# Kernel tuning notes

Hardware: AMD Instinct MI355X
Metric: run time of the kernel (lower is better)

The kernel has to match this reference:

```python
import jax, jax.numpy as jnp
import numpy as np

N = 1_000_000
C = 128
NBINS = 15


def setup_inputs() -> dict:
    key = jax.random.key(0)
    k1, k2 = jax.random.split(key)
    logits = jax.random.normal(k1, (N, C), dtype=jnp.float32)
    labels = jax.random.randint(k2, (N,), 0, C, dtype=jnp.int64)
    return {"logits": logits, "labels": labels}


def reference(logits, labels):
    n = logits.shape[0]
    probs = jax.nn.softmax(logits, axis=1)
    confidences = jnp.max(probs, axis=1)                      # [N]
    predictions = jnp.argmax(probs, axis=1)                   # [N]
    accuracies = (predictions == labels).astype(jnp.float32)  # [N]

    # Equal-count (adaptive) bin edges: interp(linspace(0,N,nbins+1), arange(N), sort(conf))
    sorted_conf = jnp.sort(confidences)
    q = jnp.linspace(0.0, float(n), NBINS + 1)
    edges = jnp.interp(q, jnp.arange(n, dtype=jnp.float32), sorted_conf)  # [NBINS+1]

    # Bin i covers (edges[i], edges[i+1]] to match conf.gt(lower) & conf.le(upper).
    idx = jnp.searchsorted(edges[1:-1], confidences, side="left")  # [N] in [0, NBINS-1]
    valid = (confidences > edges[0]) & (confidences <= edges[-1])
    idx = jnp.where(valid, idx, NBINS)  # dump out-of-range into extra segment

    cnt = jax.ops.segment_sum(jnp.ones_like(confidences), idx, num_segments=NBINS + 1)[:NBINS]
    csum = jax.ops.segment_sum(confidences, idx, num_segments=NBINS + 1)[:NBINS]
    asum = jax.ops.segment_sum(accuracies, idx, num_segments=NBINS + 1)[:NBINS]

    prop = cnt / jnp.float32(n)
    safe = jnp.maximum(cnt, 1.0)
    gap = jnp.abs(csum / safe - asum / safe)
    ece = jnp.sum(jnp.where(cnt > 0, gap * prop, 0.0))
    return ece.reshape(1)
```

## Files before the change

kernel.cpp:

```cpp
#include <hip/hip_runtime.h>
#include <hip/hip_bf16.h>
#include <cstdint>

#define NROWS 1000000
#define NCLS  128
#define NBINS 15

#define FBASE 0x3B000000u
#define NB    73728
#define SCAN_T 1024
#define PER   (NB / SCAN_T)

#define OFF_CONF   0u
#define OFF_ACC    4000000u
#define OFF_HIST   5000000u
#define OFF_SUB    5294912u
#define OFF_BINS   5417792u
#define OFF_TGTB   5418152u
#define OFF_TGTL   5418272u
#define OFF_EDGES  5418392u
#define ZERO_BYTES (OFF_TGTB - OFF_HIST)

#define ROWS_PER_BLOCK 32

__device__ __forceinline__ void reduce_row(float4 v0, float4 v1, int l16,
                                           float& c_out, int& mi_out)
{
    const int b0 = l16 * 4, b1 = 64 + l16 * 4;
    float m = v0.x; int mi = b0;
    if (v0.y > m) { m = v0.y; mi = b0 + 1; }
    if (v0.z > m) { m = v0.z; mi = b0 + 2; }
    if (v0.w > m) { m = v0.w; mi = b0 + 3; }
    if (v1.x > m) { m = v1.x; mi = b1; }
    if (v1.y > m) { m = v1.y; mi = b1 + 1; }
    if (v1.z > m) { m = v1.z; mi = b1 + 2; }
    if (v1.w > m) { m = v1.w; mi = b1 + 3; }
#pragma unroll
    for (int d = 1; d < 16; d <<= 1) {
        float om = __shfl_xor(m, d);
        int   oi = __shfl_xor(mi, d);
        if (om > m || (om == m && oi < mi)) { m = om; mi = oi; }
    }
    float s = __expf(v0.x - m) + __expf(v0.y - m) + __expf(v0.z - m) + __expf(v0.w - m)
            + __expf(v1.x - m) + __expf(v1.y - m) + __expf(v1.z - m) + __expf(v1.w - m);
#pragma unroll
    for (int d = 1; d < 16; d <<= 1) s += __shfl_xor(s, d);
    c_out  = 1.0f / s;
    mi_out = mi;
}

__global__ __launch_bounds__(256) void k_row(const float* __restrict__ logits,
                                             const int* __restrict__ labels,
                                             float* __restrict__ conf,
                                             unsigned char* __restrict__ acc,
                                             unsigned int* __restrict__ hist)
{
    const int wave = threadIdx.x >> 6;
    const int lane = threadIdx.x & 63;
    const int sub  = lane >> 4;
    const int l16  = lane & 15;
    const long long base = (long long)blockIdx.x * ROWS_PER_BLOCK + wave * 8;
    const long long rowA = base + sub;
    const long long rowB = base + 4 + sub;

    const float4* pA = reinterpret_cast<const float4*>(logits + rowA * NCLS);
    const float4* pB = reinterpret_cast<const float4*>(logits + rowB * NCLS);
    const float4 a0 = pA[l16];
    const float4 a1 = pA[16 + l16];
    const float4 b0 = pB[l16];
    const float4 b1 = pB[16 + l16];
    const int labA = labels[rowA];
    const int labB = labels[rowB];

    float cA, cB; int miA, miB;
    reduce_row(a0, a1, l16, cA, miA);
    reduce_row(b0, b1, l16, cB, miB);

    if (l16 == 0) {
        conf[rowA] = cA;
        acc[rowA]  = (labA == miA) ? 1u : 0u;
        int ubA = (int)(__float_as_uint(cA) - FBASE);
        int bA  = ubA >> 10;
        bA = bA < 0 ? 0 : (bA >= NB ? NB - 1 : bA);
        atomicAdd(&hist[bA], 1u);

        conf[rowB] = cB;
        acc[rowB]  = (labB == miB) ? 1u : 0u;
        int ubB = (int)(__float_as_uint(cB) - FBASE);
        int bB  = ubB >> 10;
        bB = bB < 0 ? 0 : (bB >= NB ? NB - 1 : bB);
        atomicAdd(&hist[bB], 1u);
    }
}

__device__ __forceinline__ unsigned int rank_of(int s)
{
    if (s == 0)  return 0u;
    if (s == 29) return (unsigned int)(NROWS - 1);
    int i = (s + 1) >> 1;
    unsigned int k = (unsigned int)((long long)i * NROWS / 15);
    return k + ((s & 1) ? 0u : 1u);
}

__global__ __launch_bounds__(SCAN_T) void k_scan(const unsigned int* __restrict__ hist,
                                                 int* __restrict__ tgtb,
                                                 int* __restrict__ tgtl)
{
    __shared__ unsigned int v[SCAN_T];
    const int t = threadIdx.x;
    unsigned int s = 0;
    for (int j = 0; j < PER; j++) s += hist[t * PER + j];
    v[t] = s;
    __syncthreads();
    for (int off = 1; off < SCAN_T; off <<= 1) {
        unsigned int x = (t >= off) ? v[t - off] : 0u;
        __syncthreads();
        v[t] += x;
        __syncthreads();
    }
    const unsigned int run0 = v[t] - s;
    for (int s2 = 0; s2 < 30; s2++) {
        unsigned int r = rank_of(s2);
        if (r >= run0 && r < run0 + s) {
            unsigned int run = run0;
            for (int j = 0; j < PER; j++) {
                unsigned int c = hist[t * PER + j];
                if (r < run + c) { tgtb[s2] = t * PER + j; tgtl[s2] = (int)(r - run); break; }
                run += c;
            }
        }
    }
}

__global__ __launch_bounds__(256) void k_subhist(const float* __restrict__ conf,
                                                 const int* __restrict__ tgtb,
                                                 unsigned int* __restrict__ sub)
{
    __shared__ int tb[30];
    if (threadIdx.x < 30) tb[threadIdx.x] = tgtb[threadIdx.x];
    __syncthreads();
    const int stride = gridDim.x * blockDim.x;
    for (int i = blockIdx.x * blockDim.x + threadIdx.x; i < NROWS / 4; i += stride) {
        float4 c4 = reinterpret_cast<const float4*>(conf)[i];
        float cv[4] = {c4.x, c4.y, c4.z, c4.w};
#pragma unroll
        for (int e = 0; e < 4; e++) {
            int ub = (int)(__float_as_uint(cv[e]) - FBASE);
            int b  = ub >> 10;
            b = b < 0 ? 0 : (b >= NB ? NB - 1 : b);
            int lo = ub & 1023;
            for (int s = 0; s < 30; s++)
                if (b == tb[s]) atomicAdd(&sub[s * 1024 + lo], 1u);
        }
    }
}

__global__ __launch_bounds__(1024) void k_edges(const unsigned int* __restrict__ sub,
                        const int* __restrict__ tgtb,
                        const int* __restrict__ tgtl,
                        float* __restrict__ edges)
{
    __shared__ float val[32];
    const int g = threadIdx.x >> 5;
    const int k = threadIdx.x & 31;
    if (g < 30) {
        const unsigned int local = (unsigned int)tgtl[g];
        unsigned int cs[32];
        unsigned int csum = 0;
        const unsigned int* p = sub + g * 1024 + k * 32;
#pragma unroll
        for (int j = 0; j < 32; j++) { cs[j] = p[j]; csum += cs[j]; }
        unsigned int incl = csum;
#pragma unroll
        for (int off = 1; off < 32; off <<= 1) {
            unsigned int x = __shfl_up(incl, off);
            if (k >= off) incl += x;
        }
        const unsigned int excl = incl - csum;
        if (local >= excl && local < excl + csum) {
            unsigned int run = excl;
            int subidx = 0;
#pragma unroll
            for (int j = 0; j < 32; j++) {
                if (local >= run && local < run + cs[j]) subidx = k * 32 + j;
                run += cs[j];
            }
            unsigned int bits = FBASE + ((unsigned int)tgtb[g] << 10) + (unsigned int)subidx;
            val[g] = __uint_as_float(bits);
        }
    }
    __syncthreads();
    if (threadIdx.x == 0) {
        edges[0]  = val[0];
        edges[15] = val[29];
        for (int i = 1; i <= 14; i++) {
            double q = (double)i * (double)NROWS / 15.0;
            long long kk = (long long)i * NROWS / 15;
            double f = q - (double)kk;
            edges[i] = (float)((1.0 - f) * (double)val[2 * i - 1] + f * (double)val[2 * i]);
        }
    }
}

__global__ __launch_bounds__(256) void k_bin(const float* __restrict__ conf,
                                             const unsigned char* __restrict__ acc,
                                             const float* __restrict__ edges,
                                             double* __restrict__ bins)
{
    __shared__ float se[16];
    __shared__ float lc[4][16], ls[4][16], la[4][16];
    const int w = threadIdx.x >> 6;
    if (threadIdx.x < 16) se[threadIdx.x] = edges[threadIdx.x];
    if (threadIdx.x < 64) {
        int a = threadIdx.x >> 4, b = threadIdx.x & 15;
        lc[a][b] = 0.f; ls[a][b] = 0.f; la[a][b] = 0.f;
    }
    __syncthreads();
    const int stride = gridDim.x * blockDim.x;
    for (int i = blockIdx.x * blockDim.x + threadIdx.x; i < NROWS / 4; i += stride) {
        float4 c4 = reinterpret_cast<const float4*>(conf)[i];
        uchar4 a4 = reinterpret_cast<const uchar4*>(acc)[i];
        float cv[4] = {c4.x, c4.y, c4.z, c4.w};
        unsigned char av[4] = {a4.x, a4.y, a4.z, a4.w};
#pragma unroll
        for (int e = 0; e < 4; e++) {
            float v = cv[e];
            if (v > se[0] && v <= se[15]) {
                int idx = 0;
#pragma unroll
                for (int j = 1; j <= 14; j++) idx += (se[j] < v) ? 1 : 0;
                atomicAdd(&lc[w][idx], 1.0f);
                atomicAdd(&ls[w][idx], v);
                atomicAdd(&la[w][idx], (float)av[e]);
            }
        }
    }
    __syncthreads();
    if (threadIdx.x < 15) {
        int t = threadIdx.x;
        atomicAdd(&bins[t],      (double)(lc[0][t] + lc[1][t] + lc[2][t] + lc[3][t]));
        atomicAdd(&bins[15 + t], (double)(ls[0][t] + ls[1][t] + ls[2][t] + ls[3][t]));
        atomicAdd(&bins[30 + t], (double)(la[0][t] + la[1][t] + la[2][t] + la[3][t]));
    }
}

__global__ void k_final(const double* __restrict__ bins, float* __restrict__ out)
{
    if (threadIdx.x == 0 && blockIdx.x == 0) {
        double ece = 0.0;
        for (int b = 0; b < NBINS; b++) {
            double cnt = bins[b];
            if (cnt > 0.0) {
                double safe = cnt < 1.0 ? 1.0 : cnt;
                double gap  = fabs(bins[15 + b] / safe - bins[30 + b] / safe);
                ece += gap * (cnt / (double)NROWS);
            }
        }
        out[0] = (float)ece;
    }
}

extern "C" void kernel_launch(void* const* d_in, const int* in_sizes, int n_in,
                              void* d_out, int out_size, void* d_ws, size_t ws_size,
                              hipStream_t stream)
{
    const float* logits = (const float*)d_in[0];
    const int*   labels = (const int*)d_in[1];
    char* ws = (char*)d_ws;

    float*         conf  = (float*)(ws + OFF_CONF);
    unsigned char* acc   = (unsigned char*)(ws + OFF_ACC);
    unsigned int*  hist  = (unsigned int*)(ws + OFF_HIST);
    unsigned int*  sub   = (unsigned int*)(ws + OFF_SUB);
    double*        bins  = (double*)(ws + OFF_BINS);
    int*           tgtb  = (int*)(ws + OFF_TGTB);
    int*           tgtl  = (int*)(ws + OFF_TGTL);
    float*         edges = (float*)(ws + OFF_EDGES);

    hipMemsetAsync(ws + OFF_HIST, 0, ZERO_BYTES, stream);

    k_row<<<NROWS / ROWS_PER_BLOCK, 256, 0, stream>>>(logits, labels, conf, acc, hist);
    k_scan<<<1, SCAN_T, 0, stream>>>(hist, tgtb, tgtl);
    k_subhist<<<1024, 256, 0, stream>>>(conf, tgtb, sub);
    k_edges<<<1, 1024, 0, stream>>>(sub, tgtb, tgtl, edges);
    k_bin<<<1024, 256, 0, stream>>>(conf, acc, edges, bins);
    k_final<<<1, 64, 0, stream>>>(bins, (float*)d_out);
}
```

Baseline: 227.8 us.

## Process four rows per 16-lane group and fold edge/final kernels via last-block pattern

The row kernel now has each 16-lane group handle four consecutive rows. Labels are read as int4, and conf and acc are written as float4/uchar4. The edge-finding and final-reduction kernels are merged into the tails of the subhist and bin kernels, using an atomic done counter so the last block does that work. This removes two kernel launches and issues more memory loads per thread. The cost is threadfence/atomic synchronization and serialized tail work on a single block.

```diff
diff --git a/kernel.cpp b/kernel.cpp
--- a/kernel.cpp
+++ b/kernel.cpp
@@ -16,12 +16,11 @@
 #define OFF_HIST   5000000u
 #define OFF_SUB    5294912u
 #define OFF_BINS   5417792u
-#define OFF_TGTB   5418152u
-#define OFF_TGTL   5418272u
-#define OFF_EDGES  5418392u
+#define OFF_DONE   5418152u
+#define OFF_TGTB   5418168u
+#define OFF_TGTL   5418288u
+#define OFF_EDGES  5418408u
 #define ZERO_BYTES (OFF_TGTB - OFF_HIST)
-
-#define ROWS_PER_BLOCK 32
 
 __device__ __forceinline__ void reduce_row(float4 v0, float4 v1, int l16,
                                            float& c_out, int& mi_out)
@@ -49,47 +48,48 @@
     mi_out = mi;
 }
 
+__device__ __forceinline__ int bucket_of(float c)
+{
+    int ub = (int)(__float_as_uint(c) - FBASE);
+    int b  = ub >> 10;
+    return b < 0 ? 0 : (b >= NB ? NB - 1 : b);
+}
+
 __global__ __launch_bounds__(256) void k_row(const float* __restrict__ logits,
                                              const int* __restrict__ labels,
                                              float* __restrict__ conf,
                                              unsigned char* __restrict__ acc,
                                              unsigned int* __restrict__ hist)
 {
-    const int wave = threadIdx.x >> 6;
-    const int lane = threadIdx.x & 63;
-    const int sub  = lane >> 4;
-    const int l16  = lane & 15;
-    const long long base = (long long)blockIdx.x * ROWS_PER_BLOCK + wave * 8;
-    const long long rowA = base + sub;
-    const long long rowB = base + 4 + sub;
-
-    const float4* pA = reinterpret_cast<const float4*>(logits + rowA * NCLS);
-    const float4* pB = reinterpret_cast<const float4*>(logits + rowB * NCLS);
-    const float4 a0 = pA[l16];
-    const float4 a1 = pA[16 + l16];
-    const float4 b0 = pB[l16];
-    const float4 b1 = pB[16 + l16];
-    const int labA = labels[rowA];
-    const int labB = labels[rowB];
-
-    float cA, cB; int miA, miB;
-    reduce_row(a0, a1, l16, cA, miA);
-    reduce_row(b0, b1, l16, cB, miB);
+    const int g   = threadIdx.x >> 4;
+    const int l16 = threadIdx.x & 15;
+    const long long row0 = (long long)blockIdx.x * 64 + g * 4;
+
+    const float4* p = reinterpret_cast<const float4*>(logits) + row0 * (NCLS / 4) + l16;
+    const float4 v0a = p[0],  v0b = p[16];
+    const float4 v1a = p[32], v1b = p[48];
+    const float4 v2a = p[64], v2b = p[80];
+    const float4 v3a = p[96], v3b = p[112];
+    const int4 lab = *reinterpret_cast<const int4*>(labels + row0);
+
+    float c0, c1, c2, c3; int m0, m1, m2, m3;
+    reduce_row(v0a, v0b, l16, c0, m0);
+    reduce_row(v1a, v1b, l16, c1, m1);
+    reduce_row(v2a, v2b, l16, c2, m2);
+    reduce_row(v3a, v3b, l16, c3, m3);
 
     if (l16 == 0) {
-        conf[rowA] = cA;
-        acc[rowA]  = (labA == miA) ? 1u : 0u;
-        int ubA = (int)(__float_as_uint(cA) - FBASE);
-        int bA  = ubA >> 10;
-        bA = bA < 0 ? 0 : (bA >= NB ? NB - 1 : bA);
-        atomicAdd(&hist[bA], 1u);
-
-        conf[rowB] = cB;
-        acc[rowB]  = (labB == miB) ? 1u : 0u;
-        int ubB = (int)(__float_as_uint(cB) - FBASE);
-        int bB  = ubB >> 10;
-        bB = bB < 0 ? 0 : (bB >= NB ? NB - 1 : bB);
-        atomicAdd(&hist[bB], 1u);
+        *reinterpret_cast<float4*>(conf + row0) = make_float4(c0, c1, c2, c3);
+        uchar4 a;
+        a.x = (lab.x == m0) ? 1 : 0;
+        a.y = (lab.y == m1) ? 1 : 0;
+        a.z = (lab.z == m2) ? 1 : 0;
+        a.w = (lab.w == m3) ? 1 : 0;
+        *reinterpret_cast<uchar4*>(acc + row0) = a;
+        atomicAdd(&hist[bucket_of(c0)], 1u);
+        atomicAdd(&hist[bucket_of(c1)], 1u);
+        atomicAdd(&hist[bucket_of(c2)], 1u);
+        atomicAdd(&hist[bucket_of(c3)], 1u);
     }
 }
 
@@ -134,7 +134,10 @@
 
 __global__ __launch_bounds__(256) void k_subhist(const float* __restrict__ conf,
                                                  const int* __restrict__ tgtb,
-                                                 unsigned int* __restrict__ sub)
+                                                 const int* __restrict__ tgtl,
+                                                 unsigned int* __restrict__ sub,
+                                                 float* __restrict__ edges,
+                                                 unsigned int* __restrict__ done)
 {
     __shared__ int tb[30];
     if (threadIdx.x < 30) tb[threadIdx.x] = tgtb[threadIdx.x];
@@ -153,23 +156,26 @@
                 if (b == tb[s]) atomicAdd(&sub[s * 1024 + lo], 1u);
         }
     }
-}
-
-__global__ __launch_bounds__(1024) void k_edges(const unsigned int* __restrict__ sub,
-                        const int* __restrict__ tgtb,
-                        const int* __restrict__ tgtl,
-                        float* __restrict__ edges)
-{
+
+    __syncthreads();
+    __shared__ unsigned int isLast;
+    if (threadIdx.x == 0) {
+        __threadfence();
+        isLast = (atomicAdd(done, 1u) == gridDim.x - 1) ? 1u : 0u;
+    }
+    __syncthreads();
+    if (!isLast) return;
+    __threadfence();
+
     __shared__ float val[32];
-    const int g = threadIdx.x >> 5;
     const int k = threadIdx.x & 31;
-    if (g < 30) {
-        const unsigned int local = (unsigned int)tgtl[g];
+    for (int slot = threadIdx.x >> 5; slot < 30; slot += 8) {
+        const unsigned int local = (unsigned int)tgtl[slot];
         unsigned int cs[32];
         unsigned int csum = 0;
-        const unsigned int* p = sub + g * 1024 + k * 32;
-#pragma unroll
-        for (int j = 0; j < 32; j++) { cs[j] = p[j]; csum += cs[j]; }
+        const unsigned int* q = sub + slot * 1024 + k * 32;
+#pragma unroll
+        for (int j = 0; j < 32; j++) { cs[j] = q[j]; csum += cs[j]; }
         unsigned int incl = csum;
 #pragma unroll
         for (int off = 1; off < 32; off <<= 1) {
@@ -185,8 +191,8 @@
                 if (local >= run && local < run + cs[j]) subidx = k * 32 + j;
                 run += cs[j];
             }
-            unsigned int bits = FBASE + ((unsigned int)tgtb[g] << 10) + (unsigned int)subidx;
-            val[g] = __uint_as_float(bits);
+            unsigned int bits = FBASE + ((unsigned int)tb[slot] << 10) + (unsigned int)subidx;
+            val[slot] = __uint_as_float(bits);
         }
     }
     __syncthreads();
@@ -205,7 +211,9 @@
 __global__ __launch_bounds__(256) void k_bin(const float* __restrict__ conf,
                                              const unsigned char* __restrict__ acc,
                                              const float* __restrict__ edges,
-                                             double* __restrict__ bins)
+                                             double* __restrict__ bins,
+                                             unsigned int* __restrict__ done,
+                                             float* __restrict__ out)
 {
     __shared__ float se[16];
     __shared__ float lc[4][16], ls[4][16], la[4][16];
@@ -242,11 +250,16 @@
         atomicAdd(&bins[15 + t], (double)(ls[0][t] + ls[1][t] + ls[2][t] + ls[3][t]));
         atomicAdd(&bins[30 + t], (double)(la[0][t] + la[1][t] + la[2][t] + la[3][t]));
     }
-}
-
-__global__ void k_final(const double* __restrict__ bins, float* __restrict__ out)
-{
-    if (threadIdx.x == 0 && blockIdx.x == 0) {
+
+    __syncthreads();
+    __shared__ unsigned int isLast;
+    if (threadIdx.x == 0) {
+        __threadfence();
+        isLast = (atomicAdd(done, 1u) == gridDim.x - 1) ? 1u : 0u;
+    }
+    __syncthreads();
+    if (isLast && threadIdx.x == 0) {
+        __threadfence();
         double ece = 0.0;
         for (int b = 0; b < NBINS; b++) {
             double cnt = bins[b];
@@ -273,16 +286,15 @@
     unsigned int*  hist  = (unsigned int*)(ws + OFF_HIST);
     unsigned int*  sub   = (unsigned int*)(ws + OFF_SUB);
     double*        bins  = (double*)(ws + OFF_BINS);
+    unsigned int*  done  = (unsigned int*)(ws + OFF_DONE);
     int*           tgtb  = (int*)(ws + OFF_TGTB);
     int*           tgtl  = (int*)(ws + OFF_TGTL);
     float*         edges = (float*)(ws + OFF_EDGES);
 
     hipMemsetAsync(ws + OFF_HIST, 0, ZERO_BYTES, stream);
 
-    k_row<<<NROWS / ROWS_PER_BLOCK, 256, 0, stream>>>(logits, labels, conf, acc, hist);
+    k_row<<<NROWS / 64, 256, 0, stream>>>(logits, labels, conf, acc, hist);
     k_scan<<<1, SCAN_T, 0, stream>>>(hist, tgtb, tgtl);
-    k_subhist<<<1024, 256, 0, stream>>>(conf, tgtb, sub);
-    k_edges<<<1, 1024, 0, stream>>>(sub, tgtb, tgtl, edges);
-    k_bin<<<1024, 256, 0, stream>>>(conf, acc, edges, bins);
-    k_final<<<1, 64, 0, stream>>>(bins, (float*)d_out);
-}
+    k_subhist<<<1024, 256, 0, stream>>>(conf, tgtb, tgtl, sub, edges, done);
+    k_bin<<<1024, 256, 0, stream>>>(conf, acc, edges, bins, done + 1, (float*)d_out);
+}
```

After: 255.2 us. +12.0%, slower.
